# Kernel optimization log

Hardware: AMD Instinct MI355X
Metric: run time of the kernel (lower is better)

## Reference

```python
import jax, jax.numpy as jnp
import numpy as np

B, R, N = 4, 1024, 100
REG_FG_THRESH = 0.55
EPS = 1e-8


def _cross2(a, b):
    return a[..., 0] * b[..., 1] - a[..., 1] * b[..., 0]


def _corners_bev(box):
    # box: (7,) [x,y,z,dx,dy,dz,heading] -> (4,2) CCW BEV corners
    x, y, dx, dy, ang = box[0], box[1], box[3], box[4], box[6]
    c, s = jnp.cos(ang), jnp.sin(ang)
    lx = jnp.array([0.5, -0.5, -0.5, 0.5], dtype=box.dtype) * dx
    ly = jnp.array([0.5, 0.5, -0.5, -0.5], dtype=box.dtype) * dy
    return jnp.stack([x + lx * c - ly * s, y + lx * s + ly * c], axis=-1)


def _points_in_box(pts, box):
    # pts (P,2), box (7,) -> (P,) bool; transform into box frame
    c, s = jnp.cos(box[6]), jnp.sin(box[6])
    px = pts[:, 0] - box[0]
    py = pts[:, 1] - box[1]
    lx = px * c + py * s
    ly = -px * s + py * c
    return (jnp.abs(lx) <= box[3] * 0.5 + 1e-5) & (jnp.abs(ly) <= box[4] * 0.5 + 1e-5)


def _bev_inter_area(boxa, boxb):
    # exact rotated-rectangle intersection area (convex polygon of <=8 verts)
    ca = _corners_bev(boxa)
    cb = _corners_bev(boxb)
    in_b = _points_in_box(ca, boxb)
    in_a = _points_in_box(cb, boxa)
    a1, a2 = ca, jnp.roll(ca, -1, axis=0)
    b1, b2 = cb, jnp.roll(cb, -1, axis=0)
    d1 = a2 - a1
    d2 = b2 - b1
    denom = _cross2(d1[:, None, :], d2[None, :, :])              # (4,4)
    diff = b1[None, :, :] - a1[:, None, :]                       # (4,4,2)
    safe = jnp.where(jnp.abs(denom) > EPS, denom, EPS)
    t = _cross2(diff, d2[None, :, :]) / safe
    u = _cross2(diff, d1[:, None, :]) / safe
    hit = (jnp.abs(denom) > EPS) & (t >= 0) & (t <= 1) & (u >= 0) & (u <= 1)
    pin = a1[:, None, :] + t[..., None] * d1[:, None, :]         # (4,4,2)
    pts = jnp.concatenate([ca, cb, pin.reshape(16, 2)], axis=0)  # (24,2)
    val = jnp.concatenate([in_b, in_a, hit.reshape(16)], axis=0)
    nv = val.sum()
    ctr = (pts * val[:, None]).sum(0) / jnp.maximum(nv, 1)
    ang = jnp.where(val, jnp.arctan2(pts[:, 1] - ctr[1], pts[:, 0] - ctr[0]), 1e9)
    order = jnp.argsort(ang)
    p = pts[order]
    v = val[order]
    first = p[0]
    p = jnp.where(v[:, None], p, first)   # pad invalid slots with first vertex (zero shoelace contribution)
    q = jnp.roll(p, -1, axis=0)
    area = 0.5 * jnp.abs(jnp.sum(p[:, 0] * q[:, 1] - q[:, 0] * p[:, 1]))
    return jnp.where(nv >= 3, area, jnp.zeros((), dtype=pts.dtype))


def _iou3d_pair(a, b):
    # same math as iou3d_nms_utils.boxes_iou3d_gpu for one pair
    inter_bev = _bev_inter_area(a, b)
    oh = jnp.clip(jnp.minimum(a[2] + a[5] * 0.5, b[2] + b[5] * 0.5)
                  - jnp.maximum(a[2] - a[5] * 0.5, b[2] - b[5] * 0.5), 0.0)
    inter = inter_bev * oh
    va = a[3] * a[4] * a[5]
    vb = b[3] * b[4] * b[5]
    return inter / jnp.clip(va + vb - inter, 1e-6, None)


_iou_rois_gts = jax.vmap(jax.vmap(_iou3d_pair, in_axes=(None, 0)), in_axes=(0, None))  # (R,N)
_iou_batched = jax.vmap(_iou_rois_gts)                                                  # (B,R,N)


def setup_inputs() -> dict:
    key = jax.random.key(0)
    ks = jax.random.split(key, 9)
    xy = jax.random.uniform(ks[0], (B, N, 2), minval=-40.0, maxval=40.0)
    z = jax.random.uniform(ks[1], (B, N, 1), minval=-2.0, maxval=0.0)
    dims = jax.random.uniform(ks[2], (B, N, 3), minval=1.0, maxval=4.5)
    heading = jax.random.uniform(ks[3], (B, N, 1), minval=-np.pi, maxval=np.pi)
    labels = jax.random.randint(ks[4], (B, N, 1), 1, 4).astype(jnp.float32)
    gt_boxes = jnp.concatenate([xy, z, dims, heading, labels], axis=-1)  # (B,N,8)
    # sampling ROIs are jittered GT boxes, mirroring generate_sampling_roi
    base_idx = jax.random.randint(ks[5], (B, R), 0, N)
    base = jnp.take_along_axis(gt_boxes[..., :7], base_idx[..., None], axis=1)  # (B,R,7)
    ctr_off = jax.random.uniform(ks[6], (B, R, 3), minval=-0.5, maxval=0.5) * base[..., 3:6]
    scale = jax.random.uniform(ks[7], (B, R, 3), minval=0.8, maxval=1.25)
    ang_off = jax.random.uniform(ks[8], (B, R, 1), minval=-np.pi / 4, maxval=np.pi / 4)
    sampling_rois = jnp.concatenate(
        [base[..., :3] + ctr_off, base[..., 3:6] * scale, base[..., 6:7] + ang_off], axis=-1)
    sampling_rois_labels = jnp.take_along_axis(gt_boxes[..., 7], base_idx, axis=1).astype(jnp.int32)
    return {"sampling_rois": sampling_rois,
            "sampling_rois_labels": sampling_rois_labels,
            "gt_boxes": gt_boxes}


def reference(sampling_rois, sampling_rois_labels, gt_boxes):
    # sample_rois_for_rcnn core: all-pairs rotated 3D IoU, best-GT assignment,
    # gather gt_of_rois, then forward()'s reg_valid_mask thresholding.
    iou3d = _iou_batched(sampling_rois, gt_boxes[..., :7])        # (B,R,N)
    max_overlaps = iou3d.max(axis=-1)                             # (B,R)
    gt_assignment = iou3d.argmax(axis=-1)                         # (B,R)
    gt_of_rois = jnp.take_along_axis(gt_boxes, gt_assignment[..., None], axis=1)  # (B,R,8)
    reg_valid_mask = (max_overlaps > REG_FG_THRESH).astype(jnp.int32)
    return sampling_rois, gt_of_rois, max_overlaps, sampling_rois_labels, reg_valid_mask
```

## Files before the change

kernel.cpp:

```cpp
#include <hip/hip_runtime.h>
#include <math.h>

#define BB 4
#define RR 1024
#define NN 100
#define NROI (BB * RR)
#define RPB 4
#define NBLK (NROI / RPB)

#define INIT_PACK 0x00000000FFFFFFFFull

__device__ __forceinline__ void corner_of(int i, float cx0, float cy0, float dx, float dy,
                                          float c, float s, float& X, float& Y) {
    float sx = (i == 0 || i == 3) ? 0.5f : -0.5f;
    float sy = (i <= 1) ? 0.5f : -0.5f;
    float lx = sx * dx, ly = sy * dy;
    X = cx0 + lx * c - ly * s;
    Y = cy0 + lx * s + ly * c;
}

__global__ __launch_bounds__(256) void sampling_target_fused(
    const float* __restrict__ rois,
    const int*   __restrict__ labels,
    const float* __restrict__ gts,
    float*       __restrict__ out)
{
    __shared__ unsigned long long s_best[8];

    const int tid  = threadIdx.x;
    const int roi0 = blockIdx.x * RPB;
    const int b    = roi0 >> 10;
    const int g    = tid >> 5;
    const int lane = tid & 31;
    const int half = g & 1;
    const int rl   = g >> 1;
    const int h    = g & 1;
    const int r    = roi0 + rl;

    const float* A = &rois[r * 7];
    float ax = A[0], ay = A[1], az = A[2], adx = A[3], ady = A[4], adz = A[5], aang = A[6];
    float acs = cosf(aang), asn = sinf(aang);
    float ra  = 0.5f * sqrtf(adx * adx + ady * ady);
    float azl = az - adz * 0.5f, azh = az + adz * 0.5f;
    float va  = adx * ady * adz;

    unsigned long long best = INIT_PACK;

    for (int r2 = 0; r2 < 2; ++r2) {
        int local = r2 * 32 + lane;
        int n     = h * 50 + local;
        bool valid = (local < 50);

        float4 g0 = make_float4(0.f, 0.f, 0.f, 0.f);
        float4 g1 = make_float4(0.f, 0.f, 0.f, 0.f);
        if (valid) {
            const float4* G = (const float4*)&gts[(b * NN + n) * 8];
            g0 = G[0];
            g1 = G[1];
        }
        float gc = cosf(g1.z), gs = sinf(g1.z);

        float ohz = fminf(azh, g0.z + g1.y * 0.5f) - fmaxf(azl, g0.z - g1.y * 0.5f);
        float dxc = ax - g0.x, dyc = ay - g0.y;
        float rsum = ra + 0.5f * sqrtf(g0.w * g0.w + g1.x * g1.x);
        bool hit = valid && (ohz > 0.0f) && (dxc * dxc + dyc * dyc <= rsum * rsum);

        unsigned long long m = __ballot(hit);
        unsigned gm = (unsigned)(half ? (m >> 32) : (m & 0xFFFFFFFFull));

        while (gm) {
            int j = __ffs(gm) - 1;
            gm &= gm - 1;

            float gx_ = __shfl(g0.x, j, 32);
            float gy_ = __shfl(g0.y, j, 32);
            float gz_ = __shfl(g0.z, j, 32);
            float gdx = __shfl(g0.w, j, 32);
            float gdy = __shfl(g1.x, j, 32);
            float gdz = __shfl(g1.y, j, 32);
            float bcs = __shfl(gc, j, 32);
            float bsn = __shfl(gs, j, 32);
            int   nj  = h * 50 + r2 * 32 + j;

            float ppx = 0.0f, ppy = 0.0f;
            bool val = false;
            if (lane < 4) {
                corner_of(lane, ax, ay, adx, ady, acs, asn, ppx, ppy);
                float qx = ppx - gx_, qy = ppy - gy_;
                float lx = qx * bcs + qy * bsn;
                float ly = -qx * bsn + qy * bcs;
                val = (fabsf(lx) <= gdx * 0.5f + 1e-5f) && (fabsf(ly) <= gdy * 0.5f + 1e-5f);
            } else if (lane < 8) {
                corner_of(lane - 4, gx_, gy_, gdx, gdy, bcs, bsn, ppx, ppy);
                float qx = ppx - ax, qy = ppy - ay;
                float lx = qx * acs + qy * asn;
                float ly = -qx * asn + qy * acs;
                val = (fabsf(lx) <= adx * 0.5f + 1e-5f) && (fabsf(ly) <= ady * 0.5f + 1e-5f);
            } else if (lane < 24) {
                int e = lane - 8;
                int ii = e >> 2, jj = e & 3;
                float a1x, a1y, a2x, a2y, b1x, b1y, b2x, b2y;
                corner_of(ii, ax, ay, adx, ady, acs, asn, a1x, a1y);
                corner_of((ii + 1) & 3, ax, ay, adx, ady, acs, asn, a2x, a2y);
                corner_of(jj, gx_, gy_, gdx, gdy, bcs, bsn, b1x, b1y);
                corner_of((jj + 1) & 3, gx_, gy_, gdx, gdy, bcs, bsn, b2x, b2y);
                float d1x = a2x - a1x, d1y = a2y - a1y;
                float d2x = b2x - b1x, d2y = b2y - b1y;
                float denom = d1x * d2y - d1y * d2x;
                float fx = b1x - a1x, fy = b1y - a1y;
                float safe = (fabsf(denom) > 1e-8f) ? denom : 1e-8f;
                float t = (fx * d2y - fy * d2x) / safe;
                float u = (fx * d1y - fy * d1x) / safe;
                ppx = a1x + t * d1x;
                ppy = a1y + t * d1y;
                val = (fabsf(denom) > 1e-8f) && (t >= 0.0f) && (t <= 1.0f) && (u >= 0.0f) && (u <= 1.0f);
            }

            unsigned long long mv = __ballot(val);
            unsigned gv = (unsigned)(half ? (mv >> 32) : (mv & 0xFFFFFFFFull));
            int nv = __popc(gv);

            float inter_bev = 0.0f;
            if (nv >= 3) {
                float sx = val ? ppx : 0.0f;
                float sy = val ? ppy : 0.0f;
#pragma unroll
                for (int off = 16; off; off >>= 1) {
                    sx += __shfl_xor(sx, off, 32);
                    sy += __shfl_xor(sy, off, 32);
                }
                float cx = sx / (float)nv, cy = sy / (float)nv;

                float dxp = ppx - cx, dyp = ppy - cy;
                float den = fabsf(dxp) + fabsf(dyp);
                float pa = dxp / fmaxf(den, 1e-30f);
                float myAng = val ? copysignf(1.0f - pa, dyp) : 1e9f;

                float sAng = 1e30f; int sIdx = 0; bool found = false;
                float gAng = 1e30f; int gIdx = 0;
#pragma unroll
                for (int jx = 0; jx < 24; jx++) {
                    float aj = __shfl(myAng, jx, 32);
                    if (aj < 1e8f) {
                        bool greater = (aj > myAng) || (aj == myAng && jx > lane);
                        if (greater && aj < sAng) { sAng = aj; sIdx = jx; found = true; }
                        if (aj < gAng) { gAng = aj; gIdx = jx; }
                    }
                }
                int qi = found ? sIdx : gIdx;
                float qx = __shfl(ppx, qi, 32);
                float qy = __shfl(ppy, qi, 32);
                float contrib = val ? (ppx * qy - qx * ppy) : 0.0f;
#pragma unroll
                for (int off = 16; off; off >>= 1)
                    contrib += __shfl_xor(contrib, off, 32);
                inter_bev = 0.5f * fabsf(contrib);
            }

            float ohp = fminf(azh, gz_ + gdz * 0.5f) - fmaxf(azl, gz_ - gdz * 0.5f);
            float inter = inter_bev * ohp;
            float vb = gdx * gdy * gdz;
            float v = inter / fmaxf(va + vb - inter, 1e-6f);
            unsigned long long packed =
                ((unsigned long long)__float_as_uint(v) << 32) | (unsigned)(~(unsigned)nj);
            best = (packed > best) ? packed : best;
        }
    }

    if (lane == 0) s_best[g] = best;
    __syncthreads();

    float* out_rois = out;
    float* out_gor  = out + NROI * 7;
    float* out_max  = out_gor + NROI * 8;
    float* out_lab  = out_max + NROI;
    float* out_msk  = out_lab + NROI;

    if (tid < RPB * 7)
        out_rois[roi0 * 7 + tid] = rois[roi0 * 7 + tid];

    if (tid < RPB) {
        unsigned long long p0 = s_best[2 * tid];
        unsigned long long p1 = s_best[2 * tid + 1];
        unsigned long long packed = (p0 > p1) ? p0 : p1;
        float mo = __uint_as_float((unsigned)(packed >> 32));
        int besti = (int)(~(unsigned)(packed & 0xFFFFFFFFu));

        int rr_ = roi0 + tid;
        const float4* G = (const float4*)&gts[(b * NN + besti) * 8];
        float4 q0 = G[0];
        float4 q1 = G[1];
        float4* og = (float4*)&out_gor[rr_ * 8];
        og[0] = q0;
        og[1] = q1;

        out_max[rr_] = mo;
        out_lab[rr_] = (float)labels[rr_];
        out_msk[rr_] = (mo > 0.55f) ? 1.0f : 0.0f;
    }
}

extern "C" void kernel_launch(void* const* d_in, const int* in_sizes, int n_in,
                              void* d_out, int out_size, void* d_ws, size_t ws_size,
                              hipStream_t stream) {
    const float* rois   = (const float*)d_in[0];
    const int*   labels = (const int*)d_in[1];
    const float* gts    = (const float*)d_in[2];
    float* out = (float*)d_out;

    hipLaunchKernelGGL(sampling_target_fused, dim3(NBLK), dim3(256), 0, stream,
                       rois, labels, gts, out);
}
```

Baseline: 71.01 us.

## Give each 64-lane wavefront one ROI and split candidate GTs across its halves

Each ROI now gets a full 64-lane wavefront instead of two 32-lane groups. The 100 GTs are prefiltered in two 64-wide ballots, and the pop loop takes two candidates per iteration, one for each 32-lane half, so both halves stay busy. The final reduction across the halves uses a wave shuffle instead of shared memory and __syncthreads, and the ROI copy and label output move to per-wave lanes. This aims to balance hit-walk work across the halves and remove block-level sync. The cost is more divergence if the hit counts are odd, plus 64-wide shuffles.

After: 69.45 us. -2.2%, faster.

```diff
diff --git a/kernel.cpp b/kernel.cpp
--- a/kernel.cpp
+++ b/kernel.cpp
@@ -19,23 +19,143 @@
     Y = cy0 + lx * s + ly * c;
 }
 
+__device__ __forceinline__ unsigned long long walk_stage(
+    unsigned long long m, int nbase,
+    float4 g0, float4 g1, float gc, float gs,
+    float ax, float ay, float azl, float azh,
+    float adx, float ady, float acs, float asn, float va,
+    int lane, int half, unsigned long long best)
+{
+    while (m) {
+        int j0 = __ffsll(m) - 1; m &= m - 1;
+        int j1 = -1;
+        if (m) { j1 = __ffsll(m) - 1; m &= m - 1; }
+        int j = half ? j1 : j0;
+        bool active = (j >= 0);
+        int js = active ? j : 0;
+
+        float gx_ = __shfl(g0.x, js, 64);
+        float gy_ = __shfl(g0.y, js, 64);
+        float gz_ = __shfl(g0.z, js, 64);
+        float gdx = __shfl(g0.w, js, 64);
+        float gdy = __shfl(g1.x, js, 64);
+        float gdz = __shfl(g1.y, js, 64);
+        float bcs = __shfl(gc, js, 64);
+        float bsn = __shfl(gs, js, 64);
+
+        float ppx = 0.0f, ppy = 0.0f;
+        bool val = false;
+        if (lane < 4) {
+            corner_of(lane, ax, ay, adx, ady, acs, asn, ppx, ppy);
+            float qx = ppx - gx_, qy = ppy - gy_;
+            float lx = qx * bcs + qy * bsn;
+            float ly = -qx * bsn + qy * bcs;
+            val = (fabsf(lx) <= gdx * 0.5f + 1e-5f) && (fabsf(ly) <= gdy * 0.5f + 1e-5f);
+        } else if (lane < 8) {
+            corner_of(lane - 4, gx_, gy_, gdx, gdy, bcs, bsn, ppx, ppy);
+            float qx = ppx - ax, qy = ppy - ay;
+            float lx = qx * acs + qy * asn;
+            float ly = -qx * asn + qy * acs;
+            val = (fabsf(lx) <= adx * 0.5f + 1e-5f) && (fabsf(ly) <= ady * 0.5f + 1e-5f);
+        } else if (lane < 24) {
+            int e = lane - 8;
+            int ii = e >> 2, jj = e & 3;
+            float a1x, a1y, a2x, a2y, b1x, b1y, b2x, b2y;
+            corner_of(ii, ax, ay, adx, ady, acs, asn, a1x, a1y);
+            corner_of((ii + 1) & 3, ax, ay, adx, ady, acs, asn, a2x, a2y);
+            corner_of(jj, gx_, gy_, gdx, gdy, bcs, bsn, b1x, b1y);
+            corner_of((jj + 1) & 3, gx_, gy_, gdx, gdy, bcs, bsn, b2x, b2y);
+            float d1x = a2x - a1x, d1y = a2y - a1y;
+            float d2x = b2x - b1x, d2y = b2y - b1y;
+            float denom = d1x * d2y - d1y * d2x;
+            float fx = b1x - a1x, fy = b1y - a1y;
+            float safe = (fabsf(denom) > 1e-8f) ? denom : 1e-8f;
+            float t = (fx * d2y - fy * d2x) / safe;
+            float u = (fx * d1y - fy * d1x) / safe;
+            ppx = a1x + t * d1x;
+            ppy = a1y + t * d1y;
+            val = (fabsf(denom) > 1e-8f) && (t >= 0.0f) && (t <= 1.0f) && (u >= 0.0f) && (u <= 1.0f);
+        }
+        val = val && active;
+
+        unsigned long long mv = __ballot(val);
+        unsigned gv = (unsigned)(half ? (mv >> 32) : (mv & 0xFFFFFFFFull));
+        int nv = __popc(gv);
+
+        float inter_bev = 0.0f;
+        if (nv >= 3) {
+            float sx = val ? ppx : 0.0f;
+            float sy = val ? ppy : 0.0f;
+#pragma unroll
+            for (int off = 16; off; off >>= 1) {
+                sx += __shfl_xor(sx, off, 32);
+                sy += __shfl_xor(sy, off, 32);
+            }
+            float cx = sx / (float)nv, cy = sy / (float)nv;
+
+            float dxp = ppx - cx, dyp = ppy - cy;
+            float den = fabsf(dxp) + fabsf(dyp);
+            float pa = dxp / fmaxf(den, 1e-30f);
+            float myAng = val ? copysignf(1.0f - pa, dyp) : 1e9f;
+
+            float sAng = 1e30f; int sIdx = 0; bool found = false;
+            float gAng = 1e30f; int gIdx = 0;
+#pragma unroll
+            for (int jx = 0; jx < 24; jx++) {
+                float aj = __shfl(myAng, jx, 32);
+                if (aj < 1e8f) {
+                    bool greater = (aj > myAng) || (aj == myAng && jx > lane);
+                    if (greater && aj < sAng) { sAng = aj; sIdx = jx; found = true; }
+                    if (aj < gAng) { gAng = aj; gIdx = jx; }
+                }
+            }
+            int qi = found ? sIdx : gIdx;
+            float qx = __shfl(ppx, qi, 32);
+            float qy = __shfl(ppy, qi, 32);
+            float contrib = val ? (ppx * qy - qx * ppy) : 0.0f;
+#pragma unroll
+            for (int off = 16; off; off >>= 1)
+                contrib += __shfl_xor(contrib, off, 32);
+            inter_bev = 0.5f * fabsf(contrib);
+        }
+
+        if (active) {
+            float ohp = fminf(azh, gz_ + gdz * 0.5f) - fmaxf(azl, gz_ - gdz * 0.5f);
+            float inter = inter_bev * ohp;
+            float vb = gdx * gdy * gdz;
+            float v = inter / fmaxf(va + vb - inter, 1e-6f);
+            int nj = nbase + j;
+            unsigned long long packed =
+                ((unsigned long long)__float_as_uint(v) << 32) | (unsigned)(~(unsigned)nj);
+            best = (packed > best) ? packed : best;
+        }
+    }
+    return best;
+}
+
 __global__ __launch_bounds__(256) void sampling_target_fused(
     const float* __restrict__ rois,
     const int*   __restrict__ labels,
     const float* __restrict__ gts,
     float*       __restrict__ out)
 {
-    __shared__ unsigned long long s_best[8];
-
     const int tid  = threadIdx.x;
+    const int w    = tid >> 6;
+    const int wl   = tid & 63;
+    const int lane = tid & 31;
+    const int half = (tid >> 5) & 1;
     const int roi0 = blockIdx.x * RPB;
+    const int r    = roi0 + w;
     const int b    = roi0 >> 10;
-    const int g    = tid >> 5;
-    const int lane = tid & 31;
-    const int half = g & 1;
-    const int rl   = g >> 1;
-    const int h    = g & 1;
-    const int r    = roi0 + rl;
+
+    float* out_rois = out;
+    float* out_gor  = out + NROI * 7;
+    float* out_max  = out_gor + NROI * 8;
+    float* out_lab  = out_max + NROI;
+    float* out_msk  = out_lab + NROI;
+
+    if (wl < 7) out_rois[r * 7 + wl] = rois[r * 7 + wl];
+    if (wl == 7) out_lab[r] = (float)labels[r];
 
     const float* A = &rois[r * 7];
     float ax = A[0], ay = A[1], az = A[2], adx = A[3], ady = A[4], adz = A[5], aang = A[6];
@@ -44,159 +164,62 @@
     float azl = az - adz * 0.5f, azh = az + adz * 0.5f;
     float va  = adx * ady * adz;
 
+    const int n1 = 64 + wl;
+    const bool v1 = (n1 < NN);
+    const float4* G0 = (const float4*)&gts[(b * NN + wl) * 8];
+    float4 a0 = G0[0];
+    float4 a1 = G0[1];
+    float4 c0 = make_float4(0.f, 0.f, 0.f, 0.f);
+    float4 c1 = make_float4(0.f, 0.f, 0.f, 0.f);
+    if (v1) {
+        const float4* G1 = (const float4*)&gts[(b * NN + n1) * 8];
+        c0 = G1[0];
+        c1 = G1[1];
+    }
+    float gc0 = cosf(a1.z), gs0 = sinf(a1.z);
+    float gc1 = cosf(c1.z), gs1 = sinf(c1.z);
+
+    float oh0 = fminf(azh, a0.z + a1.y * 0.5f) - fmaxf(azl, a0.z - a1.y * 0.5f);
+    float dx0 = ax - a0.x, dy0 = ay - a0.y;
+    float rs0 = ra + 0.5f * sqrtf(a0.w * a0.w + a1.x * a1.x);
+    bool hit0 = (oh0 > 0.0f) && (dx0 * dx0 + dy0 * dy0 <= rs0 * rs0);
+
+    float oh1 = fminf(azh, c0.z + c1.y * 0.5f) - fmaxf(azl, c0.z - c1.y * 0.5f);
+    float dx1 = ax - c0.x, dy1 = ay - c0.y;
+    float rs1 = ra + 0.5f * sqrtf(c0.w * c0.w + c1.x * c1.x);
+    bool hit1 = v1 && (oh1 > 0.0f) && (dx1 * dx1 + dy1 * dy1 <= rs1 * rs1);
+
+    unsigned long long m0 = __ballot(hit0);
+    unsigned long long m1 = __ballot(hit1);
+
     unsigned long long best = INIT_PACK;
-
-    for (int r2 = 0; r2 < 2; ++r2) {
-        int local = r2 * 32 + lane;
-        int n     = h * 50 + local;
-        bool valid = (local < 50);
-
-        float4 g0 = make_float4(0.f, 0.f, 0.f, 0.f);
-        float4 g1 = make_float4(0.f, 0.f, 0.f, 0.f);
-        if (valid) {
-            const float4* G = (const float4*)&gts[(b * NN + n) * 8];
-            g0 = G[0];
-            g1 = G[1];
-        }
-        float gc = cosf(g1.z), gs = sinf(g1.z);
-
-        float ohz = fminf(azh, g0.z + g1.y * 0.5f) - fmaxf(azl, g0.z - g1.y * 0.5f);
-        float dxc = ax - g0.x, dyc = ay - g0.y;
-        float rsum = ra + 0.5f * sqrtf(g0.w * g0.w + g1.x * g1.x);
-        bool hit = valid && (ohz > 0.0f) && (dxc * dxc + dyc * dyc <= rsum * rsum);
-
-        unsigned long long m = __ballot(hit);
-        unsigned gm = (unsigned)(half ? (m >> 32) : (m & 0xFFFFFFFFull));
-
-        while (gm) {
-            int j = __ffs(gm) - 1;
-            gm &= gm - 1;
-
-            float gx_ = __shfl(g0.x, j, 32);
-            float gy_ = __shfl(g0.y, j, 32);
-            float gz_ = __shfl(g0.z, j, 32);
-            float gdx = __shfl(g0.w, j, 32);
-            float gdy = __shfl(g1.x, j, 32);
-            float gdz = __shfl(g1.y, j, 32);
-            float bcs = __shfl(gc, j, 32);
-            float bsn = __shfl(gs, j, 32);
-            int   nj  = h * 50 + r2 * 32 + j;
-
-            float ppx = 0.0f, ppy = 0.0f;
-            bool val = false;
-            if (lane < 4) {
-                corner_of(lane, ax, ay, adx, ady, acs, asn, ppx, ppy);
-                float qx = ppx - gx_, qy = ppy - gy_;
-                float lx = qx * bcs + qy * bsn;
-                float ly = -qx * bsn + qy * bcs;
-                val = (fabsf(lx) <= gdx * 0.5f + 1e-5f) && (fabsf(ly) <= gdy * 0.5f + 1e-5f);
-            } else if (lane < 8) {
-                corner_of(lane - 4, gx_, gy_, gdx, gdy, bcs, bsn, ppx, ppy);
-                float qx = ppx - ax, qy = ppy - ay;
-                float lx = qx * acs + qy * asn;
-                float ly = -qx * asn + qy * acs;
-                val = (fabsf(lx) <= adx * 0.5f + 1e-5f) && (fabsf(ly) <= ady * 0.5f + 1e-5f);
-            } else if (lane < 24) {
-                int e = lane - 8;
-                int ii = e >> 2, jj = e & 3;
-                float a1x, a1y, a2x, a2y, b1x, b1y, b2x, b2y;
-                corner_of(ii, ax, ay, adx, ady, acs, asn, a1x, a1y);
-                corner_of((ii + 1) & 3, ax, ay, adx, ady, acs, asn, a2x, a2y);
-                corner_of(jj, gx_, gy_, gdx, gdy, bcs, bsn, b1x, b1y);
-                corner_of((jj + 1) & 3, gx_, gy_, gdx, gdy, bcs, bsn, b2x, b2y);
-                float d1x = a2x - a1x, d1y = a2y - a1y;
-                float d2x = b2x - b1x, d2y = b2y - b1y;
-                float denom = d1x * d2y - d1y * d2x;
-                float fx = b1x - a1x, fy = b1y - a1y;
-                float safe = (fabsf(denom) > 1e-8f) ? denom : 1e-8f;
-                float t = (fx * d2y - fy * d2x) / safe;
-                float u = (fx * d1y - fy * d1x) / safe;
-                ppx = a1x + t * d1x;
-                ppy = a1y + t * d1y;
-                val = (fabsf(denom) > 1e-8f) && (t >= 0.0f) && (t <= 1.0f) && (u >= 0.0f) && (u <= 1.0f);
-            }
-
-            unsigned long long mv = __ballot(val);
-            unsigned gv = (unsigned)(half ? (mv >> 32) : (mv & 0xFFFFFFFFull));
-            int nv = __popc(gv);
-
-            float inter_bev = 0.0f;
-            if (nv >= 3) {
-                float sx = val ? ppx : 0.0f;
-                float sy = val ? ppy : 0.0f;
-#pragma unroll
-                for (int off = 16; off; off >>= 1) {
-                    sx += __shfl_xor(sx, off, 32);
-                    sy += __shfl_xor(sy, off, 32);
-                }
-                float cx = sx / (float)nv, cy = sy / (float)nv;
-
-                float dxp = ppx - cx, dyp = ppy - cy;
-                float den = fabsf(dxp) + fabsf(dyp);
-                float pa = dxp / fmaxf(den, 1e-30f);
-                float myAng = val ? copysignf(1.0f - pa, dyp) : 1e9f;
-
-                float sAng = 1e30f; int sIdx = 0; bool found = false;
-                float gAng = 1e30f; int gIdx = 0;
-#pragma unroll
-                for (int jx = 0; jx < 24; jx++) {
-                    float aj = __shfl(myAng, jx, 32);
-                    if (aj < 1e8f) {
-                        bool greater = (aj > myAng) || (aj == myAng && jx > lane);
-                        if (greater && aj < sAng) { sAng = aj; sIdx = jx; found = true; }
-                        if (aj < gAng) { gAng = aj; gIdx = jx; }
-                    }
-                }
-                int qi = found ? sIdx : gIdx;
-                float qx = __shfl(ppx, qi, 32);
-                float qy = __shfl(ppy, qi, 32);
-                float contrib = val ? (ppx * qy - qx * ppy) : 0.0f;
-#pragma unroll
-                for (int off = 16; off; off >>= 1)
-                    contrib += __shfl_xor(contrib, off, 32);
-                inter_bev = 0.5f * fabsf(contrib);
-            }
-
-            float ohp = fminf(azh, gz_ + gdz * 0.5f) - fmaxf(azl, gz_ - gdz * 0.5f);
-            float inter = inter_bev * ohp;
-            float vb = gdx * gdy * gdz;
-            float v = inter / fmaxf(va + vb - inter, 1e-6f);
-            unsigned long long packed =
-                ((unsigned long long)__float_as_uint(v) << 32) | (unsigned)(~(unsigned)nj);
-            best = (packed > best) ? packed : best;
-        }
-    }
-
-    if (lane == 0) s_best[g] = best;
-    __syncthreads();
-
-    float* out_rois = out;
-    float* out_gor  = out + NROI * 7;
-    float* out_max  = out_gor + NROI * 8;
-    float* out_lab  = out_max + NROI;
-    float* out_msk  = out_lab + NROI;
-
-    if (tid < RPB * 7)
-        out_rois[roi0 * 7 + tid] = rois[roi0 * 7 + tid];
-
-    if (tid < RPB) {
-        unsigned long long p0 = s_best[2 * tid];
-        unsigned long long p1 = s_best[2 * tid + 1];
-        unsigned long long packed = (p0 > p1) ? p0 : p1;
-        float mo = __uint_as_float((unsigned)(packed >> 32));
-        int besti = (int)(~(unsigned)(packed & 0xFFFFFFFFu));
-
-        int rr_ = roi0 + tid;
+    best = walk_stage(m0, 0,  a0, a1, gc0, gs0,
+                      ax, ay, azl, azh, adx, ady, acs, asn, va, lane, half, best);
+    best = walk_stage(m1, 64, c0, c1, gc1, gs1,
+                      ax, ay, azl, azh, adx, ady, acs, asn, va, lane, half, best);
+
+    {
+        int p = wl ^ 32;
+        unsigned bl = (unsigned)best, bh = (unsigned)(best >> 32);
+        unsigned ol = (unsigned)__shfl((int)bl, p, 64);
+        unsigned oh_ = (unsigned)__shfl((int)bh, p, 64);
+        unsigned long long other = ((unsigned long long)oh_ << 32) | ol;
+        best = (other > best) ? other : best;
+    }
+
+    if (wl == 0) {
+        float mo = __uint_as_float((unsigned)(best >> 32));
+        int besti = (int)(~(unsigned)(best & 0xFFFFFFFFu));
+
         const float4* G = (const float4*)&gts[(b * NN + besti) * 8];
         float4 q0 = G[0];
         float4 q1 = G[1];
-        float4* og = (float4*)&out_gor[rr_ * 8];
+        float4* og = (float4*)&out_gor[r * 8];
         og[0] = q0;
         og[1] = q1;
 
-        out_max[rr_] = mo;
-        out_lab[rr_] = (float)labels[rr_];
-        out_msk[rr_] = (mo > 0.55f) ? 1.0f : 0.0f;
+        out_max[r] = mo;
+        out_msk[r] = (mo > 0.55f) ? 1.0f : 0.0f;
     }
 }
 
```
